# Optimization experiments

Hardware: AMD Instinct MI355X
Metric: run time of the kernel (lower is better)

## Reference

```python
import jax, jax.numpy as jnp
import numpy as np

EPS = 1e-5  # torch LayerNorm default
DT = 0.01   # ODE resolution
H = 8       # num_heads

def layernorm(x, g, b):
    m = jnp.mean(x, axis=-1, keepdims=True)
    v = jnp.mean(jnp.square(x - m), axis=-1, keepdims=True)
    return (x - m) * jax.lax.rsqrt(v + EPS) * g + b


def setup_inputs() -> dict:
    key = jax.random.key(0)
    ks = jax.random.split(key, 16)
    B, N, C = 8, 256, 256
    s = 0.02
    x = jax.random.normal(ks[0], (B, N, C), dtype=jnp.float32)
    # lead times as integer hundredths (== int(lead_time / 0.01)); force max = 50
    lead_times = jax.random.randint(ks[1], (B,), 10, 51, dtype=jnp.int32).at[0].set(50)
    return {
        "x": x,
        "wqkv": jax.random.normal(ks[2], (C, 3 * C), jnp.float32) * s,
        "bqkv": jnp.zeros((3 * C,), jnp.float32),
        "wo": jax.random.normal(ks[3], (C, C), jnp.float32) * s,
        "bo": jnp.zeros((C,), jnp.float32),
        "g1": jnp.ones((C,), jnp.float32),
        "b1": jnp.zeros((C,), jnp.float32),
        "g2": jnp.ones((C,), jnp.float32),
        "b2": jnp.zeros((C,), jnp.float32),
        "wl1": jax.random.normal(ks[4], (C, C), jnp.float32) * s,
        "bl1": jnp.zeros((C,), jnp.float32),
        "wl2": jax.random.normal(ks[5], (C, C), jnp.float32) * s,
        "bl2": jnp.zeros((C,), jnp.float32),
        "gn": jnp.ones((C,), jnp.float32),
        "bn": jnp.zeros((C,), jnp.float32),
        "lead_times": lead_times,
        "n_steps": 50,
    }


def reference(x, wqkv, bqkv, wo, bo, g1, b1, g2, b2, wl1, bl1, wl2, bl2, gn, bn,
              lead_times, n_steps):
    B, N, C = x.shape
    hd = C // H
    scale = 1.0 / (hd ** 0.5)

    # --- ContinuousAttention (eval mode: dropout = identity). Note: the source
    # computes a cross-image attention but overwrites it, so only the per-patch
    # attention contributes to the output. ---
    qkv = (x @ wqkv + bqkv).reshape(B, N, 3, H, hd).transpose(2, 0, 3, 1, 4)
    q, k, v = qkv[0], qkv[1], qkv[2]                  # [B,H,N,hd]
    scores = jnp.einsum('bhqd,bhkd->bhqk', q, k) * scale
    attn = jax.nn.softmax(scores, axis=-1)
    po = jnp.einsum('bhqk,bhkd->bhqd', attn, v)       # [B,H,N,hd]
    attn_out = po.transpose(0, 2, 1, 3).reshape(B, N, C) @ wo + bo

    x1 = layernorm(x + attn_out, g1, b1)

    # --- ODE func: LN(lin2(relu(lin1(y))) + y) ---
    def f(y):
        h = jax.nn.relu(y @ wl1 + bl1) @ wl2 + bl2
        return layernorm(h + y, gn, bn)

    # torchdiffeq 'rk4' = fixed-step 3/8-rule RK4
    def step(y, _):
        k1 = f(y)
        k2 = f(y + DT * k1 * (1.0 / 3.0))
        k3 = f(y + DT * (k2 - k1 * (1.0 / 3.0)))
        k4 = f(y + DT * (k1 - k2 + k3))
        yn = y + DT * 0.125 * (k1 + 3.0 * (k2 + k3) + k4)
        return yn, yn

    _, traj = jax.lax.scan(step, x1, None, length=n_steps)
    traj = jnp.concatenate([x1[None], traj], axis=0)  # [n_steps+1, B, N, C]

    idx = lead_times.astype(jnp.int32)                # step indices
    ode_out = traj[idx, jnp.arange(B)]                # [B, N, C]

    return layernorm(x1 + ode_out, g2, b2)
```

## Files before the change

### kernel.cpp

```cpp
#include <hip/hip_runtime.h>
#include <math.h>

#define CDIM 256
#define NHEAD 8
#define HD 32
#define BSZ 8
#define NTOK 256
#define MROWS (BSZ*NTOK)
#define LN_EPS 1e-5f
#define DT_STEP 0.01f

template<int R>
__device__ __forceinline__ void ln_stats(const float* val, int tid,
        float (*part_s)[R], float (*part_q)[R], float* mb, float* rb) {
    const int lane = tid & 63;
    const int wid  = tid >> 6;
    #pragma unroll
    for (int r = 0; r < R; ++r) {
        float s = val[r];
        float q = val[r] * val[r];
        #pragma unroll
        for (int off = 32; off > 0; off >>= 1) {
            s += __shfl_down(s, off, 64);
            q += __shfl_down(q, off, 64);
        }
        if (lane == 0) { part_s[wid][r] = s; part_q[wid][r] = q; }
    }
    __syncthreads();
    if (tid < R) {
        float S = part_s[0][tid] + part_s[1][tid] + part_s[2][tid] + part_s[3][tid];
        float Q = part_q[0][tid] + part_q[1][tid] + part_q[2][tid] + part_q[3][tid];
        float mean = S * (1.0f / CDIM);
        float var  = Q * (1.0f / CDIM) - mean * mean;
        mb[tid] = mean;
        rb[tid] = rsqrtf(var + LN_EPS);
    }
    __syncthreads();
}

__global__ __launch_bounds__(256) void qkv_kernel(
        const float* __restrict__ X, const float* __restrict__ W,
        const float* __restrict__ bias, float* __restrict__ OUT) {
    const int R = 8;
    __shared__ float xs[R][CDIM];
    const int base = blockIdx.x * R;
    const int tid = threadIdx.x;
    #pragma unroll
    for (int r = 0; r < R; ++r) xs[r][tid] = X[(size_t)(base + r) * CDIM + tid];
    __syncthreads();
    for (int g = 0; g < 3; ++g) {
        const int j = g * 256 + tid;
        float acc[R];
        #pragma unroll
        for (int r = 0; r < R; ++r) acc[r] = 0.0f;
        const float* wp = W + j;
        for (int k = 0; k < CDIM; k += 4) {
            float w0 = wp[(size_t)(k+0)*768];
            float w1 = wp[(size_t)(k+1)*768];
            float w2 = wp[(size_t)(k+2)*768];
            float w3 = wp[(size_t)(k+3)*768];
            #pragma unroll
            for (int r = 0; r < R; ++r) {
                float4 xv = *reinterpret_cast<const float4*>(&xs[r][k]);
                acc[r] = fmaf(xv.x, w0, acc[r]);
                acc[r] = fmaf(xv.y, w1, acc[r]);
                acc[r] = fmaf(xv.z, w2, acc[r]);
                acc[r] = fmaf(xv.w, w3, acc[r]);
            }
        }
        const float bb = bias[j];
        #pragma unroll
        for (int r = 0; r < R; ++r) OUT[(size_t)(base + r) * 768 + j] = acc[r] + bb;
    }
}

__global__ __launch_bounds__(256) void attn_kernel(
        const float* __restrict__ QKV, float* __restrict__ PO) {
    __shared__ float ks[NTOK][HD];
    __shared__ float vs[NTOK][HD];
    const int bh = blockIdx.x;
    const int b = bh >> 3;
    const int h = bh & 7;
    const int tid = threadIdx.x;
    for (int idx = tid; idx < NTOK * HD; idx += 256) {
        const int j = idx >> 5;
        const int d = idx & 31;
        const float* row = QKV + (size_t)(b * NTOK + j) * 768 + h * HD + d;
        ks[j][d] = row[256];
        vs[j][d] = row[512];
    }
    __syncthreads();
    float q[HD];
    const float* qrow = QKV + (size_t)(b * NTOK + tid) * 768 + h * HD;
    #pragma unroll
    for (int d = 0; d < HD; ++d) q[d] = qrow[d];
    const float scale = 0.17677669529663687f;
    float m = -1e30f, l = 0.0f;
    float po[HD];
    #pragma unroll
    for (int d = 0; d < HD; ++d) po[d] = 0.0f;
    for (int j = 0; j < NTOK; ++j) {
        float s = 0.0f;
        #pragma unroll
        for (int d = 0; d < HD; ++d) s = fmaf(q[d], ks[j][d], s);
        s *= scale;
        const float nm = fmaxf(m, s);
        const float corr = __expf(m - nm);
        const float p = __expf(s - nm);
        l = l * corr + p;
        #pragma unroll
        for (int d = 0; d < HD; ++d) po[d] = fmaf(po[d], corr, p * vs[j][d]);
        m = nm;
    }
    const float inv = 1.0f / l;
    float* dst = PO + (size_t)(b * NTOK + tid) * CDIM + h * HD;
    #pragma unroll
    for (int d = 0; d < HD; ++d) dst[d] = po[d] * inv;
}

__global__ __launch_bounds__(256) void oproj_ln_kernel(
        const float* __restrict__ PO, const float* __restrict__ WO,
        const float* __restrict__ BO, const float* __restrict__ X,
        const float* __restrict__ G1, const float* __restrict__ B1,
        float* __restrict__ X1) {
    const int R = 8;
    __shared__ float ps[R][CDIM];
    __shared__ float part_s[4][R], part_q[4][R];
    __shared__ float mb[R], rb[R];
    const int base = blockIdx.x * R;
    const int tid = threadIdx.x;
    #pragma unroll
    for (int r = 0; r < R; ++r) ps[r][tid] = PO[(size_t)(base + r) * CDIM + tid];
    __syncthreads();
    float acc[R];
    #pragma unroll
    for (int r = 0; r < R; ++r) acc[r] = 0.0f;
    const float* wp = WO + tid;
    for (int k = 0; k < CDIM; k += 4) {
        float w0 = wp[(size_t)(k+0)*CDIM];
        float w1 = wp[(size_t)(k+1)*CDIM];
        float w2 = wp[(size_t)(k+2)*CDIM];
        float w3 = wp[(size_t)(k+3)*CDIM];
        #pragma unroll
        for (int r = 0; r < R; ++r) {
            float4 xv = *reinterpret_cast<const float4*>(&ps[r][k]);
            acc[r] = fmaf(xv.x, w0, acc[r]);
            acc[r] = fmaf(xv.y, w1, acc[r]);
            acc[r] = fmaf(xv.z, w2, acc[r]);
            acc[r] = fmaf(xv.w, w3, acc[r]);
        }
    }
    const float bo = BO[tid];
    float val[R];
    #pragma unroll
    for (int r = 0; r < R; ++r)
        val[r] = acc[r] + bo + X[(size_t)(base + r) * CDIM + tid];
    ln_stats<R>(val, tid, part_s, part_q, mb, rb);
    const float g = G1[tid], bb = B1[tid];
    #pragma unroll
    for (int r = 0; r < R; ++r)
        X1[(size_t)(base + r) * CDIM + tid] = (val[r] - mb[r]) * rb[r] * g + bb;
}

struct OdeShared {
    float bufA[8][CDIM];
    float bufB[8][CDIM];
    float red[4][8][CDIM];
    float pS[16][2], pQ[16][2];
};

__device__ __forceinline__ unsigned int bf16_rne(float x) {
    unsigned int u = __float_as_uint(x);
    return (u + 0x7FFFu + ((u >> 16) & 1u)) >> 16;
}

__device__ __forceinline__ void gemv_slice_p(
        const float (*buf)[CDIM], int k0, const uint4* wv, float* acc) {
    #pragma unroll
    for (int c = 0; c < 8; ++c) {
        const uint4 pv = wv[c];
        const float w0 = __uint_as_float(pv.x << 16);
        const float w1 = __uint_as_float(pv.x & 0xFFFF0000u);
        const float w2 = __uint_as_float(pv.y << 16);
        const float w3 = __uint_as_float(pv.y & 0xFFFF0000u);
        const float w4 = __uint_as_float(pv.z << 16);
        const float w5 = __uint_as_float(pv.z & 0xFFFF0000u);
        const float w6 = __uint_as_float(pv.w << 16);
        const float w7 = __uint_as_float(pv.w & 0xFFFF0000u);
        #pragma unroll
        for (int r = 0; r < 8; ++r) {
            const float4 x0 = *reinterpret_cast<const float4*>(&buf[r][k0 + 8*c]);
            const float4 x1 = *reinterpret_cast<const float4*>(&buf[r][k0 + 8*c + 4]);
            acc[r] = fmaf(x0.x, w0, acc[r]);
            acc[r] = fmaf(x0.y, w1, acc[r]);
            acc[r] = fmaf(x0.z, w2, acc[r]);
            acc[r] = fmaf(x0.w, w3, acc[r]);
            acc[r] = fmaf(x1.x, w4, acc[r]);
            acc[r] = fmaf(x1.y, w5, acc[r]);
            acc[r] = fmaf(x1.z, w6, acc[r]);
            acc[r] = fmaf(x1.w, w7, acc[r]);
        }
    }
}

__device__ __forceinline__ void ode_feval(
        float a0, float a1, float& o0, float& o1,
        int col, int kq, int lane, int wid,
        const uint4* w1v, const uint4* w2v,
        float bl1, float bl2, float gnv, float bnv, OdeShared& sh) {
    const int r0 = kq * 2;
    const int k0 = kq * 64;
    sh.bufA[r0][col]     = a0;
    sh.bufA[r0 + 1][col] = a1;
    __syncthreads();

    float acc[8];
    #pragma unroll
    for (int r = 0; r < 8; ++r) acc[r] = 0.0f;
    gemv_slice_p(sh.bufA, k0, w1v, acc);
    #pragma unroll
    for (int r = 0; r < 8; ++r) sh.red[kq][r][col] = acc[r];
    __syncthreads();

    {
        float h0 = sh.red[0][r0][col] + sh.red[1][r0][col]
                 + sh.red[2][r0][col] + sh.red[3][r0][col] + bl1;
        float h1 = sh.red[0][r0+1][col] + sh.red[1][r0+1][col]
                 + sh.red[2][r0+1][col] + sh.red[3][r0+1][col] + bl1;
        sh.bufB[r0][col]     = fmaxf(h0, 0.0f);
        sh.bufB[r0 + 1][col] = fmaxf(h1, 0.0f);
    }
    __syncthreads();

    #pragma unroll
    for (int r = 0; r < 8; ++r) acc[r] = 0.0f;
    gemv_slice_p(sh.bufB, k0, w2v, acc);
    #pragma unroll
    for (int r = 0; r < 8; ++r) sh.red[kq][r][col] = acc[r];
    __syncthreads();

    float v0 = sh.red[0][r0][col] + sh.red[1][r0][col]
             + sh.red[2][r0][col] + sh.red[3][r0][col] + bl2 + a0;
    float v1 = sh.red[0][r0+1][col] + sh.red[1][r0+1][col]
             + sh.red[2][r0+1][col] + sh.red[3][r0+1][col] + bl2 + a1;

    float s0 = v0, q0 = v0 * v0, s1 = v1, q1 = v1 * v1;
    #pragma unroll
    for (int off = 32; off > 0; off >>= 1) {
        s0 += __shfl_down(s0, off, 64);
        q0 += __shfl_down(q0, off, 64);
        s1 += __shfl_down(s1, off, 64);
        q1 += __shfl_down(q1, off, 64);
    }
    if (lane == 0) {
        sh.pS[wid][0] = s0; sh.pQ[wid][0] = q0;
        sh.pS[wid][1] = s1; sh.pQ[wid][1] = q1;
    }
    __syncthreads();
    const int wb = kq << 2;
    float S0 = sh.pS[wb][0] + sh.pS[wb+1][0] + sh.pS[wb+2][0] + sh.pS[wb+3][0];
    float Q0 = sh.pQ[wb][0] + sh.pQ[wb+1][0] + sh.pQ[wb+2][0] + sh.pQ[wb+3][0];
    float S1 = sh.pS[wb][1] + sh.pS[wb+1][1] + sh.pS[wb+2][1] + sh.pS[wb+3][1];
    float Q1 = sh.pQ[wb][1] + sh.pQ[wb+1][1] + sh.pQ[wb+2][1] + sh.pQ[wb+3][1];
    float m0 = S0 * (1.0f / CDIM);
    float m1 = S1 * (1.0f / CDIM);
    float rs0 = rsqrtf(Q0 * (1.0f / CDIM) - m0 * m0 + LN_EPS);
    float rs1 = rsqrtf(Q1 * (1.0f / CDIM) - m1 * m1 + LN_EPS);
    o0 = (v0 - m0) * rs0 * gnv + bnv;
    o1 = (v1 - m1) * rs1 * gnv + bnv;
}

__global__ __launch_bounds__(1024, 4) void ode_kernel(
        const float* __restrict__ X1,
        const float* __restrict__ WL1, const float* __restrict__ BL1,
        const float* __restrict__ WL2, const float* __restrict__ BL2,
        const float* __restrict__ GN, const float* __restrict__ BN,
        const float* __restrict__ G2, const float* __restrict__ B2,
        const int* __restrict__ LT, const int* __restrict__ NSTEP,
        float* __restrict__ OUT) {
    __shared__ OdeShared sh;
    const int t = threadIdx.x;
    const int col = t & 255;
    const int kq  = t >> 8;
    const int lane = t & 63;
    const int wid  = t >> 6;
    const int wg = blockIdx.x;
    const int b  = wg >> 5;
    const int rg = wg & 31;
    const int base = b * NTOK + rg * 8;
    int steps = LT[b];
    const int ns = NSTEP[0];
    if (steps > ns) steps = ns;

    const float bl1 = BL1[col], bl2 = BL2[col];
    const float gnv = GN[col],  bnv = BN[col];
    const int k0 = kq * 64;

    uint4 w1v[8], w2v[8];
    {
        const float* p1 = WL1 + (size_t)k0 * CDIM + col;
        const float* p2 = WL2 + (size_t)k0 * CDIM + col;
        #pragma unroll
        for (int c = 0; c < 8; ++c) {
            unsigned int u1[4], u2[4];
            #pragma unroll
            for (int q = 0; q < 4; ++q) {
                const int kk = 8 * c + 2 * q;
                float a1w = p1[(size_t)(kk)     * CDIM];
                float b1w = p1[(size_t)(kk + 1) * CDIM];
                float a2w = p2[(size_t)(kk)     * CDIM];
                float b2w = p2[(size_t)(kk + 1) * CDIM];
                u1[q] = bf16_rne(a1w) | (bf16_rne(b1w) << 16);
                u2[q] = bf16_rne(a2w) | (bf16_rne(b2w) << 16);
            }
            w1v[c] = make_uint4(u1[0], u1[1], u1[2], u1[3]);
            w2v[c] = make_uint4(u2[0], u2[1], u2[2], u2[3]);
        }
    }

    const int r0 = kq * 2;
    const float x10 = X1[(size_t)(base + r0) * CDIM + col];
    const float x11 = X1[(size_t)(base + r0 + 1) * CDIM + col];
    float y0 = x10, y1 = x11;

    for (int s = 0; s < steps; ++s) {
        float k10, k11, k20, k21, k30, k31, k40, k41, a0, a1;
        ode_feval(y0, y1, k10, k11, col, kq, lane, wid, w1v, w2v, bl1, bl2, gnv, bnv, sh);
        a0 = fmaf(DT_STEP * (1.0f/3.0f), k10, y0);
        a1 = fmaf(DT_STEP * (1.0f/3.0f), k11, y1);
        ode_feval(a0, a1, k20, k21, col, kq, lane, wid, w1v, w2v, bl1, bl2, gnv, bnv, sh);
        a0 = fmaf(DT_STEP, k20 - k10 * (1.0f/3.0f), y0);
        a1 = fmaf(DT_STEP, k21 - k11 * (1.0f/3.0f), y1);
        ode_feval(a0, a1, k30, k31, col, kq, lane, wid, w1v, w2v, bl1, bl2, gnv, bnv, sh);
        a0 = fmaf(DT_STEP, k10 - k20 + k30, y0);
        a1 = fmaf(DT_STEP, k11 - k21 + k31, y1);
        ode_feval(a0, a1, k40, k41, col, kq, lane, wid, w1v, w2v, bl1, bl2, gnv, bnv, sh);
        y0 = fmaf(DT_STEP * 0.125f, k10 + 3.0f * (k20 + k30) + k40, y0);
        y1 = fmaf(DT_STEP * 0.125f, k11 + 3.0f * (k21 + k31) + k41, y1);
    }

    float v0 = x10 + y0;
    float v1 = x11 + y1;
    float s0 = v0, q0 = v0 * v0, s1 = v1, q1 = v1 * v1;
    #pragma unroll
    for (int off = 32; off > 0; off >>= 1) {
        s0 += __shfl_down(s0, off, 64);
        q0 += __shfl_down(q0, off, 64);
        s1 += __shfl_down(s1, off, 64);
        q1 += __shfl_down(q1, off, 64);
    }
    if (lane == 0) {
        sh.pS[wid][0] = s0; sh.pQ[wid][0] = q0;
        sh.pS[wid][1] = s1; sh.pQ[wid][1] = q1;
    }
    __syncthreads();
    const int wb = kq << 2;
    float S0 = sh.pS[wb][0] + sh.pS[wb+1][0] + sh.pS[wb+2][0] + sh.pS[wb+3][0];
    float Q0 = sh.pQ[wb][0] + sh.pQ[wb+1][0] + sh.pQ[wb+2][0] + sh.pQ[wb+3][0];
    float S1 = sh.pS[wb][1] + sh.pS[wb+1][1] + sh.pS[wb+2][1] + sh.pS[wb+3][1];
    float Q1 = sh.pQ[wb][1] + sh.pQ[wb+1][1] + sh.pQ[wb+2][1] + sh.pQ[wb+3][1];
    float m0 = S0 * (1.0f / CDIM);
    float m1 = S1 * (1.0f / CDIM);
    float rs0 = rsqrtf(Q0 * (1.0f / CDIM) - m0 * m0 + LN_EPS);
    float rs1 = rsqrtf(Q1 * (1.0f / CDIM) - m1 * m1 + LN_EPS);
    const float g2 = G2[col], b2 = B2[col];
    OUT[(size_t)(base + r0) * CDIM + col]     = (v0 - m0) * rs0 * g2 + b2;
    OUT[(size_t)(base + r0 + 1) * CDIM + col] = (v1 - m1) * rs1 * g2 + b2;
}

extern "C" void kernel_launch(void* const* d_in, const int* in_sizes, int n_in,
                              void* d_out, int out_size, void* d_ws, size_t ws_size,
                              hipStream_t stream) {
    const float* x    = (const float*)d_in[0];
    const float* wqkv = (const float*)d_in[1];
    const float* bqkv = (const float*)d_in[2];
    const float* wo   = (const float*)d_in[3];
    const float* bo   = (const float*)d_in[4];
    const float* g1   = (const float*)d_in[5];
    const float* b1   = (const float*)d_in[6];
    const float* g2   = (const float*)d_in[7];
    const float* b2   = (const float*)d_in[8];
    const float* wl1  = (const float*)d_in[9];
    const float* bl1  = (const float*)d_in[10];
    const float* wl2  = (const float*)d_in[11];
    const float* bl2  = (const float*)d_in[12];
    const float* gn   = (const float*)d_in[13];
    const float* bn   = (const float*)d_in[14];
    const int*   lt   = (const int*)d_in[15];
    const int*   nst  = (const int*)d_in[16];

    float* ws  = (float*)d_ws;
    float* qkv = ws;
    float* po  = qkv + (size_t)MROWS * 768;
    float* x1  = po  + (size_t)MROWS * CDIM;
    float* out = (float*)d_out;

    hipLaunchKernelGGL(qkv_kernel, dim3(MROWS / 8), dim3(256), 0, stream,
                       x, wqkv, bqkv, qkv);
    hipLaunchKernelGGL(attn_kernel, dim3(BSZ * NHEAD), dim3(256), 0, stream,
                       qkv, po);
    hipLaunchKernelGGL(oproj_ln_kernel, dim3(MROWS / 8), dim3(256), 0, stream,
                       po, wo, bo, x, g1, b1, x1);
    hipLaunchKernelGGL(ode_kernel, dim3(MROWS / 8), dim3(1024), 0, stream,
                       x1, wl1, bl1, wl2, bl2, gn, bn, g2, b2, lt, nst, out);
}
```

Measured before the change: 3.416 ms.

## Stage WL1 in swizzled LDS, remap threads to interleave k-split, shuffle-reduce partials

Moves the first ODE weight matrix from per-thread registers into a 128KB swizzled bf16 LDS copy, keeping only WL2 in registers. Threads are remapped so the four k-slices of a column sit in adjacent lanes, which lets partial sums be combined with xor shuffles instead of an LDS reduction buffer and extra barriers. This removes two barriers per function evaluation and relieves register pressure. In exchange each block needs about 145KB of dynamic LDS, which limits residency to one block per CU and adds LDS weight reads inside the inner loop.

```diff
diff --git a/kernel.cpp b/kernel.cpp
--- a/kernel.cpp
+++ b/kernel.cpp
@@ -9,6 +9,8 @@
 #define MROWS (BSZ*NTOK)
 #define LN_EPS 1e-5f
 #define DT_STEP 0.01f
+
+#define ODE_LDS_BYTES 148480
 
 template<int R>
 __device__ __forceinline__ void ln_stats(const float* val, int tid,
@@ -162,115 +164,144 @@
         X1[(size_t)(base + r) * CDIM + tid] = (val[r] - mb[r]) * rb[r] * g + bb;
 }
 
-struct OdeShared {
-    float bufA[8][CDIM];
-    float bufB[8][CDIM];
-    float red[4][8][CDIM];
-    float pS[16][2], pQ[16][2];
-};
+struct WRegs { uint4 m0, m1, m2, m3, m4, m5, m6, m7; };
 
 __device__ __forceinline__ unsigned int bf16_rne(float x) {
     unsigned int u = __float_as_uint(x);
     return (u + 0x7FFFu + ((u >> 16) & 1u)) >> 16;
 }
 
-__device__ __forceinline__ void gemv_slice_p(
-        const float (*buf)[CDIM], int k0, const uint4* wv, float* acc) {
-    #pragma unroll
-    for (int c = 0; c < 8; ++c) {
-        const uint4 pv = wv[c];
-        const float w0 = __uint_as_float(pv.x << 16);
-        const float w1 = __uint_as_float(pv.x & 0xFFFF0000u);
-        const float w2 = __uint_as_float(pv.y << 16);
-        const float w3 = __uint_as_float(pv.y & 0xFFFF0000u);
-        const float w4 = __uint_as_float(pv.z << 16);
-        const float w5 = __uint_as_float(pv.z & 0xFFFF0000u);
-        const float w6 = __uint_as_float(pv.w << 16);
-        const float w7 = __uint_as_float(pv.w & 0xFFFF0000u);
-        #pragma unroll
-        for (int r = 0; r < 8; ++r) {
-            const float4 x0 = *reinterpret_cast<const float4*>(&buf[r][k0 + 8*c]);
-            const float4 x1 = *reinterpret_cast<const float4*>(&buf[r][k0 + 8*c + 4]);
-            acc[r] = fmaf(x0.x, w0, acc[r]);
-            acc[r] = fmaf(x0.y, w1, acc[r]);
-            acc[r] = fmaf(x0.z, w2, acc[r]);
-            acc[r] = fmaf(x0.w, w3, acc[r]);
-            acc[r] = fmaf(x1.x, w4, acc[r]);
-            acc[r] = fmaf(x1.y, w5, acc[r]);
-            acc[r] = fmaf(x1.z, w6, acc[r]);
-            acc[r] = fmaf(x1.w, w7, acc[r]);
-        }
+__device__ __forceinline__ uint4 pack_w(const float* pcol, int kstart) {
+    const float* p = pcol + (size_t)kstart * CDIM;
+    unsigned int u0 = bf16_rne(p[0*CDIM]) | (bf16_rne(p[1*CDIM]) << 16);
+    unsigned int u1 = bf16_rne(p[2*CDIM]) | (bf16_rne(p[3*CDIM]) << 16);
+    unsigned int u2 = bf16_rne(p[4*CDIM]) | (bf16_rne(p[5*CDIM]) << 16);
+    unsigned int u3 = bf16_rne(p[6*CDIM]) | (bf16_rne(p[7*CDIM]) << 16);
+    return make_uint4(u0, u1, u2, u3);
+}
+
+__device__ __forceinline__ void fma_chunk(
+        const float (*buf)[CDIM], int kbase, uint4 pv, float* acc) {
+    const float w0 = __uint_as_float(pv.x << 16);
+    const float w1 = __uint_as_float(pv.x & 0xFFFF0000u);
+    const float w2 = __uint_as_float(pv.y << 16);
+    const float w3 = __uint_as_float(pv.y & 0xFFFF0000u);
+    const float w4 = __uint_as_float(pv.z << 16);
+    const float w5 = __uint_as_float(pv.z & 0xFFFF0000u);
+    const float w6 = __uint_as_float(pv.w << 16);
+    const float w7 = __uint_as_float(pv.w & 0xFFFF0000u);
+    #pragma unroll
+    for (int r = 0; r < 8; ++r) {
+        const float4 x0 = *reinterpret_cast<const float4*>(&buf[r][kbase]);
+        const float4 x1 = *reinterpret_cast<const float4*>(&buf[r][kbase + 4]);
+        acc[r] = fmaf(x0.x, w0, acc[r]);
+        acc[r] = fmaf(x0.y, w1, acc[r]);
+        acc[r] = fmaf(x0.z, w2, acc[r]);
+        acc[r] = fmaf(x0.w, w3, acc[r]);
+        acc[r] = fmaf(x1.x, w4, acc[r]);
+        acc[r] = fmaf(x1.y, w5, acc[r]);
+        acc[r] = fmaf(x1.z, w6, acc[r]);
+        acc[r] = fmaf(x1.w, w7, acc[r]);
     }
 }
 
 __device__ __forceinline__ void ode_feval(
         float a0, float a1, float& o0, float& o1,
-        int col, int kq, int lane, int wid,
-        const uint4* w1v, const uint4* w2v,
-        float bl1, float bl2, float gnv, float bnv, OdeShared& sh) {
+        int col, int kq, int lane, int wid, int swz,
+        const char* smem, float (*bufA)[CDIM], float (*bufB)[CDIM],
+        float (*pS)[16], float (*pQ)[16],
+        const WRegs& w2,
+        float bl1, float bl2, float gnv, float bnv) {
     const int r0 = kq * 2;
-    const int k0 = kq * 64;
-    sh.bufA[r0][col]     = a0;
-    sh.bufA[r0 + 1][col] = a1;
+    bufA[r0][col]     = a0;
+    bufA[r0 + 1][col] = a1;
     __syncthreads();
 
     float acc[8];
     #pragma unroll
     for (int r = 0; r < 8; ++r) acc[r] = 0.0f;
-    gemv_slice_p(sh.bufA, k0, w1v, acc);
-    #pragma unroll
-    for (int r = 0; r < 8; ++r) sh.red[kq][r][col] = acc[r];
-    __syncthreads();
-
     {
-        float h0 = sh.red[0][r0][col] + sh.red[1][r0][col]
-                 + sh.red[2][r0][col] + sh.red[3][r0][col] + bl1;
-        float h1 = sh.red[0][r0+1][col] + sh.red[1][r0+1][col]
-                 + sh.red[2][r0+1][col] + sh.red[3][r0+1][col] + bl1;
-        sh.bufB[r0][col]     = fmaxf(h0, 0.0f);
-        sh.bufB[r0 + 1][col] = fmaxf(h1, 0.0f);
-    }
+        const char* w1base = smem + (col << 9);
+        #pragma unroll
+        for (int c = 0; c < 8; ++c) {
+            const int woff = ((c << 6) + (kq << 4)) ^ swz;
+            const uint4 wv = *reinterpret_cast<const uint4*>(w1base + woff);
+            fma_chunk(bufA, c * 32 + kq * 8, wv, acc);
+        }
+    }
+    #pragma unroll
+    for (int r = 0; r < 8; ++r) {
+        acc[r] += __shfl_xor(acc[r], 1, 64);
+        acc[r] += __shfl_xor(acc[r], 2, 64);
+    }
+    bufB[r0][col]     = fmaxf(acc[r0]     + bl1, 0.0f);
+    bufB[r0 + 1][col] = fmaxf(acc[r0 + 1] + bl1, 0.0f);
     __syncthreads();
 
     #pragma unroll
     for (int r = 0; r < 8; ++r) acc[r] = 0.0f;
-    gemv_slice_p(sh.bufB, k0, w2v, acc);
-    #pragma unroll
-    for (int r = 0; r < 8; ++r) sh.red[kq][r][col] = acc[r];
-    __syncthreads();
-
-    float v0 = sh.red[0][r0][col] + sh.red[1][r0][col]
-             + sh.red[2][r0][col] + sh.red[3][r0][col] + bl2 + a0;
-    float v1 = sh.red[0][r0+1][col] + sh.red[1][r0+1][col]
-             + sh.red[2][r0+1][col] + sh.red[3][r0+1][col] + bl2 + a1;
+    fma_chunk(bufB, 0 * 32 + kq * 8, w2.m0, acc);
+    fma_chunk(bufB, 1 * 32 + kq * 8, w2.m1, acc);
+    fma_chunk(bufB, 2 * 32 + kq * 8, w2.m2, acc);
+    fma_chunk(bufB, 3 * 32 + kq * 8, w2.m3, acc);
+    fma_chunk(bufB, 4 * 32 + kq * 8, w2.m4, acc);
+    fma_chunk(bufB, 5 * 32 + kq * 8, w2.m5, acc);
+    fma_chunk(bufB, 6 * 32 + kq * 8, w2.m6, acc);
+    fma_chunk(bufB, 7 * 32 + kq * 8, w2.m7, acc);
+    #pragma unroll
+    for (int r = 0; r < 8; ++r) {
+        acc[r] += __shfl_xor(acc[r], 1, 64);
+        acc[r] += __shfl_xor(acc[r], 2, 64);
+    }
+    const float v0 = acc[r0]     + bl2 + a0;
+    const float v1 = acc[r0 + 1] + bl2 + a1;
 
     float s0 = v0, q0 = v0 * v0, s1 = v1, q1 = v1 * v1;
     #pragma unroll
-    for (int off = 32; off > 0; off >>= 1) {
-        s0 += __shfl_down(s0, off, 64);
-        q0 += __shfl_down(q0, off, 64);
-        s1 += __shfl_down(s1, off, 64);
-        q1 += __shfl_down(q1, off, 64);
-    }
-    if (lane == 0) {
-        sh.pS[wid][0] = s0; sh.pQ[wid][0] = q0;
-        sh.pS[wid][1] = s1; sh.pQ[wid][1] = q1;
-    }
-    __syncthreads();
-    const int wb = kq << 2;
-    float S0 = sh.pS[wb][0] + sh.pS[wb+1][0] + sh.pS[wb+2][0] + sh.pS[wb+3][0];
-    float Q0 = sh.pQ[wb][0] + sh.pQ[wb+1][0] + sh.pQ[wb+2][0] + sh.pQ[wb+3][0];
-    float S1 = sh.pS[wb][1] + sh.pS[wb+1][1] + sh.pS[wb+2][1] + sh.pS[wb+3][1];
-    float Q1 = sh.pQ[wb][1] + sh.pQ[wb+1][1] + sh.pQ[wb+2][1] + sh.pQ[wb+3][1];
-    float m0 = S0 * (1.0f / CDIM);
-    float m1 = S1 * (1.0f / CDIM);
-    float rs0 = rsqrtf(Q0 * (1.0f / CDIM) - m0 * m0 + LN_EPS);
-    float rs1 = rsqrtf(Q1 * (1.0f / CDIM) - m1 * m1 + LN_EPS);
+    for (int off = 4; off <= 32; off <<= 1) {
+        s0 += __shfl_xor(s0, off, 64);
+        q0 += __shfl_xor(q0, off, 64);
+        s1 += __shfl_xor(s1, off, 64);
+        q1 += __shfl_xor(q1, off, 64);
+    }
+    if (lane < 4) {
+        pS[r0][wid] = s0; pQ[r0][wid] = q0;
+        pS[r0 + 1][wid] = s1; pQ[r0 + 1][wid] = q1;
+    }
+    __syncthreads();
+    float4 sA = *reinterpret_cast<const float4*>(&pS[r0][0]);
+    float4 sB = *reinterpret_cast<const float4*>(&pS[r0][4]);
+    float4 sC = *reinterpret_cast<const float4*>(&pS[r0][8]);
+    float4 sD = *reinterpret_cast<const float4*>(&pS[r0][12]);
+    float S0 = (sA.x+sA.y+sA.z+sA.w) + (sB.x+sB.y+sB.z+sB.w)
+             + (sC.x+sC.y+sC.z+sC.w) + (sD.x+sD.y+sD.z+sD.w);
+    sA = *reinterpret_cast<const float4*>(&pQ[r0][0]);
+    sB = *reinterpret_cast<const float4*>(&pQ[r0][4]);
+    sC = *reinterpret_cast<const float4*>(&pQ[r0][8]);
+    sD = *reinterpret_cast<const float4*>(&pQ[r0][12]);
+    float Q0 = (sA.x+sA.y+sA.z+sA.w) + (sB.x+sB.y+sB.z+sB.w)
+             + (sC.x+sC.y+sC.z+sC.w) + (sD.x+sD.y+sD.z+sD.w);
+    sA = *reinterpret_cast<const float4*>(&pS[r0+1][0]);
+    sB = *reinterpret_cast<const float4*>(&pS[r0+1][4]);
+    sC = *reinterpret_cast<const float4*>(&pS[r0+1][8]);
+    sD = *reinterpret_cast<const float4*>(&pS[r0+1][12]);
+    float S1 = (sA.x+sA.y+sA.z+sA.w) + (sB.x+sB.y+sB.z+sB.w)
+             + (sC.x+sC.y+sC.z+sC.w) + (sD.x+sD.y+sD.z+sD.w);
+    sA = *reinterpret_cast<const float4*>(&pQ[r0+1][0]);
+    sB = *reinterpret_cast<const float4*>(&pQ[r0+1][4]);
+    sC = *reinterpret_cast<const float4*>(&pQ[r0+1][8]);
+    sD = *reinterpret_cast<const float4*>(&pQ[r0+1][12]);
+    float Q1 = (sA.x+sA.y+sA.z+sA.w) + (sB.x+sB.y+sB.z+sB.w)
+             + (sC.x+sC.y+sC.z+sC.w) + (sD.x+sD.y+sD.z+sD.w);
+    const float m0 = S0 * (1.0f / CDIM);
+    const float m1 = S1 * (1.0f / CDIM);
+    const float rs0 = rsqrtf(Q0 * (1.0f / CDIM) - m0 * m0 + LN_EPS);
+    const float rs1 = rsqrtf(Q1 * (1.0f / CDIM) - m1 * m1 + LN_EPS);
     o0 = (v0 - m0) * rs0 * gnv + bnv;
     o1 = (v1 - m1) * rs1 * gnv + bnv;
 }
 
-__global__ __launch_bounds__(1024, 4) void ode_kernel(
+__global__ __launch_bounds__(1024) void ode_kernel(
         const float* __restrict__ X1,
         const float* __restrict__ WL1, const float* __restrict__ BL1,
         const float* __restrict__ WL2, const float* __restrict__ BL2,
@@ -278,12 +309,18 @@
         const float* __restrict__ G2, const float* __restrict__ B2,
         const int* __restrict__ LT, const int* __restrict__ NSTEP,
         float* __restrict__ OUT) {
-    __shared__ OdeShared sh;
-    const int t = threadIdx.x;
-    const int col = t & 255;
-    const int kq  = t >> 8;
+    extern __shared__ char smem[];
+    float (*bufA)[CDIM] = reinterpret_cast<float (*)[CDIM]>(smem + 131072);
+    float (*bufB)[CDIM] = reinterpret_cast<float (*)[CDIM]>(smem + 139264);
+    float (*pS)[16]     = reinterpret_cast<float (*)[16]>(smem + 147456);
+    float (*pQ)[16]     = reinterpret_cast<float (*)[16]>(smem + 147968);
+
+    const int t    = threadIdx.x;
+    const int col  = t >> 2;
+    const int kq   = t & 3;
     const int lane = t & 63;
     const int wid  = t >> 6;
+    const int swz  = (col & 7) << 4;
     const int wg = blockIdx.x;
     const int b  = wg >> 5;
     const int rg = wg & 31;
@@ -292,77 +329,77 @@
     const int ns = NSTEP[0];
     if (steps > ns) steps = ns;
 
+    for (int i = 0; i < 64; ++i) {
+        const int idx = i * 1024 + t;
+        const int k = idx >> 8;
+        const int c = idx & 255;
+        const unsigned short hv = (unsigned short)bf16_rne(WL1[idx]);
+        const int off = (c << 9) + (((k << 1)) ^ ((c & 7) << 4));
+        *reinterpret_cast<unsigned short*>(smem + off) = hv;
+    }
+    const float* p2 = WL2 + col;
+    WRegs w2;
+    w2.m0 = pack_w(p2, 0 * 32 + kq * 8);
+    w2.m1 = pack_w(p2, 1 * 32 + kq * 8);
+    w2.m2 = pack_w(p2, 2 * 32 + kq * 8);
+    w2.m3 = pack_w(p2, 3 * 32 + kq * 8);
+    w2.m4 = pack_w(p2, 4 * 32 + kq * 8);
+    w2.m5 = pack_w(p2, 5 * 32 + kq * 8);
+    w2.m6 = pack_w(p2, 6 * 32 + kq * 8);
+    w2.m7 = pack_w(p2, 7 * 32 + kq * 8);
+    __syncthreads();
+
     const float bl1 = BL1[col], bl2 = BL2[col];
     const float gnv = GN[col],  bnv = BN[col];
-    const int k0 = kq * 64;
-
-    uint4 w1v[8], w2v[8];
-    {
-        const float* p1 = WL1 + (size_t)k0 * CDIM + col;
-        const float* p2 = WL2 + (size_t)k0 * CDIM + col;
-        #pragma unroll
-        for (int c = 0; c < 8; ++c) {
-            unsigned int u1[4], u2[4];
-            #pragma unroll
-            for (int q = 0; q < 4; ++q) {
-                const int kk = 8 * c + 2 * q;
-                float a1w = p1[(size_t)(kk)     * CDIM];
-                float b1w = p1[(size_t)(kk + 1) * CDIM];
-                float a2w = p2[(size_t)(kk)     * CDIM];
-                float b2w = p2[(size_t)(kk + 1) * CDIM];
-                u1[q] = bf16_rne(a1w) | (bf16_rne(b1w) << 16);
-                u2[q] = bf16_rne(a2w) | (bf16_rne(b2w) << 16);
-            }
-            w1v[c] = make_uint4(u1[0], u1[1], u1[2], u1[3]);
-            w2v[c] = make_uint4(u2[0], u2[1], u2[2], u2[3]);
-        }
-    }
-
     const int r0 = kq * 2;
+
+    float y0 = X1[(size_t)(base + r0) * CDIM + col];
+    float y1 = X1[(size_t)(base + r0 + 1) * CDIM + col];
+
+    for (int s = 0; s < steps; ++s) {
+        float k10, k11, k20, k21, k30, k31, k40, k41, a0, a1;
+        ode_feval(y0, y1, k10, k11, col, kq, lane, wid, swz, smem, bufA, bufB, pS, pQ, w2, bl1, bl2, gnv, bnv);
+        a0 = fmaf(DT_STEP * (1.0f/3.0f), k10, y0);
+        a1 = fmaf(DT_STEP * (1.0f/3.0f), k11, y1);
+        ode_feval(a0, a1, k20, k21, col, kq, lane, wid, swz, smem, bufA, bufB, pS, pQ, w2, bl1, bl2, gnv, bnv);
+        a0 = fmaf(DT_STEP, k20 - k10 * (1.0f/3.0f), y0);
+        a1 = fmaf(DT_STEP, k21 - k11 * (1.0f/3.0f), y1);
+        ode_feval(a0, a1, k30, k31, col, kq, lane, wid, swz, smem, bufA, bufB, pS, pQ, w2, bl1, bl2, gnv, bnv);
+        a0 = fmaf(DT_STEP, k10 - k20 + k30, y0);
+        a1 = fmaf(DT_STEP, k11 - k21 + k31, y1);
+        ode_feval(a0, a1, k40, k41, col, kq, lane, wid, swz, smem, bufA, bufB, pS, pQ, w2, bl1, bl2, gnv, bnv);
+        y0 = fmaf(DT_STEP * 0.125f, k10 + 3.0f * (k20 + k30) + k40, y0);
+        y1 = fmaf(DT_STEP * 0.125f, k11 + 3.0f * (k21 + k31) + k41, y1);
+    }
+
     const float x10 = X1[(size_t)(base + r0) * CDIM + col];
     const float x11 = X1[(size_t)(base + r0 + 1) * CDIM + col];
-    float y0 = x10, y1 = x11;
-
-    for (int s = 0; s < steps; ++s) {
-        float k10, k11, k20, k21, k30, k31, k40, k41, a0, a1;
-        ode_feval(y0, y1, k10, k11, col, kq, lane, wid, w1v, w2v, bl1, bl2, gnv, bnv, sh);
-        a0 = fmaf(DT_STEP * (1.0f/3.0f), k10, y0);
-        a1 = fmaf(DT_STEP * (1.0f/3.0f), k11, y1);
-        ode_feval(a0, a1, k20, k21, col, kq, lane, wid, w1v, w2v, bl1, bl2, gnv, bnv, sh);
-        a0 = fmaf(DT_STEP, k20 - k10 * (1.0f/3.0f), y0);
-        a1 = fmaf(DT_STEP, k21 - k11 * (1.0f/3.0f), y1);
-        ode_feval(a0, a1, k30, k31, col, kq, lane, wid, w1v, w2v, bl1, bl2, gnv, bnv, sh);
-        a0 = fmaf(DT_STEP, k10 - k20 + k30, y0);
-        a1 = fmaf(DT_STEP, k11 - k21 + k31, y1);
-        ode_feval(a0, a1, k40, k41, col, kq, lane, wid, w1v, w2v, bl1, bl2, gnv, bnv, sh);
-        y0 = fmaf(DT_STEP * 0.125f, k10 + 3.0f * (k20 + k30) + k40, y0);
-        y1 = fmaf(DT_STEP * 0.125f, k11 + 3.0f * (k21 + k31) + k41, y1);
-    }
-
-    float v0 = x10 + y0;
-    float v1 = x11 + y1;
+    const float v0 = x10 + y0;
+    const float v1 = x11 + y1;
     float s0 = v0, q0 = v0 * v0, s1 = v1, q1 = v1 * v1;
     #pragma unroll
-    for (int off = 32; off > 0; off >>= 1) {
-        s0 += __shfl_down(s0, off, 64);
-        q0 += __shfl_down(q0, off, 64);
-        s1 += __shfl_down(s1, off, 64);
-        q1 += __shfl_down(q1, off, 64);
-    }
-    if (lane == 0) {
-        sh.pS[wid][0] = s0; sh.pQ[wid][0] = q0;
-        sh.pS[wid][1] = s1; sh.pQ[wid][1] = q1;
-    }
-    __syncthreads();
-    const int wb = kq << 2;
-    float S0 = sh.pS[wb][0] + sh.pS[wb+1][0] + sh.pS[wb+2][0] + sh.pS[wb+3][0];
-    float Q0 = sh.pQ[wb][0] + sh.pQ[wb+1][0] + sh.pQ[wb+2][0] + sh.pQ[wb+3][0];
-    float S1 = sh.pS[wb][1] + sh.pS[wb+1][1] + sh.pS[wb+2][1] + sh.pS[wb+3][1];
-    float Q1 = sh.pQ[wb][1] + sh.pQ[wb+1][1] + sh.pQ[wb+2][1] + sh.pQ[wb+3][1];
-    float m0 = S0 * (1.0f / CDIM);
-    float m1 = S1 * (1.0f / CDIM);
-    float rs0 = rsqrtf(Q0 * (1.0f / CDIM) - m0 * m0 + LN_EPS);
-    float rs1 = rsqrtf(Q1 * (1.0f / CDIM) - m1 * m1 + LN_EPS);
+    for (int off = 4; off <= 32; off <<= 1) {
+        s0 += __shfl_xor(s0, off, 64);
+        q0 += __shfl_xor(q0, off, 64);
+        s1 += __shfl_xor(s1, off, 64);
+        q1 += __shfl_xor(q1, off, 64);
+    }
+    __syncthreads();
+    if (lane < 4) {
+        pS[r0][wid] = s0; pQ[r0][wid] = q0;
+        pS[r0 + 1][wid] = s1; pQ[r0 + 1][wid] = q1;
+    }
+    __syncthreads();
+    float S0 = 0.0f, Q0 = 0.0f, S1 = 0.0f, Q1 = 0.0f;
+    #pragma unroll
+    for (int wv = 0; wv < 16; ++wv) {
+        S0 += pS[r0][wv];     Q0 += pQ[r0][wv];
+        S1 += pS[r0 + 1][wv]; Q1 += pQ[r0 + 1][wv];
+    }
+    const float m0 = S0 * (1.0f / CDIM);
+    const float m1 = S1 * (1.0f / CDIM);
+    const float rs0 = rsqrtf(Q0 * (1.0f / CDIM) - m0 * m0 + LN_EPS);
+    const float rs1 = rsqrtf(Q1 * (1.0f / CDIM) - m1 * m1 + LN_EPS);
     const float g2 = G2[col], b2 = B2[col];
     OUT[(size_t)(base + r0) * CDIM + col]     = (v0 - m0) * rs0 * g2 + b2;
     OUT[(size_t)(base + r0 + 1) * CDIM + col] = (v1 - m1) * rs1 * g2 + b2;
@@ -395,12 +432,16 @@
     float* x1  = po  + (size_t)MROWS * CDIM;
     float* out = (float*)d_out;
 
+    (void)hipFuncSetAttribute(reinterpret_cast<const void*>(ode_kernel),
+                              hipFuncAttributeMaxDynamicSharedMemorySize,
+                              ODE_LDS_BYTES);
+
     hipLaunchKernelGGL(qkv_kernel, dim3(MROWS / 8), dim3(256), 0, stream,
                        x, wqkv, bqkv, qkv);
     hipLaunchKernelGGL(attn_kernel, dim3(BSZ * NHEAD), dim3(256), 0, stream,
                        qkv, po);
     hipLaunchKernelGGL(oproj_ln_kernel, dim3(MROWS / 8), dim3(256), 0, stream,
                        po, wo, bo, x, g1, b1, x1);
-    hipLaunchKernelGGL(ode_kernel, dim3(MROWS / 8), dim3(1024), 0, stream,
+    hipLaunchKernelGGL(ode_kernel, dim3(MROWS / 8), dim3(1024), ODE_LDS_BYTES, stream,
                        x1, wl1, bl1, wl2, bl2, gn, bn, g2, b2, lt, nst, out);
 }
```

New measurement: 5.027 ms. +47.2%, slower.
